# Optimization experiments

Hardware: AMD Instinct MI355X
Metric: run time of the kernel (lower is better)

Reference implementation:

```python
import jax, jax.numpy as jnp
import numpy as np

B, T, K = 128, 1024, 24
START_TAG, END_TAG = 22, 23


def setup_inputs() -> dict:
    key = jax.random.key(0)
    k1, k2, k3 = jax.random.split(key, 3)
    scores = jax.random.normal(k1, (B, T, K, K), dtype=jnp.float32)
    targets = jax.random.randint(k2, (B, T), 0, K * K)
    # lengths must be sorted descending (pack_padded_sequence convention), >= 1
    lengths = jnp.sort(jax.random.randint(k3, (B,), 1, T + 1))[::-1]
    return {"scores": scores, "targets": targets, "lengths": lengths}


def reference(scores, targets, lengths):
    b, t_len, k, _ = scores.shape
    # gold path score: gather targets from flattened [B,T,K*K] view, mask by length
    flat = scores.reshape(b, t_len, k * k)
    scores_at_targets = jnp.take_along_axis(flat, targets[:, :, None], axis=2)[..., 0]  # [B,T]
    time_mask = jnp.arange(t_len)[None, :] < lengths[:, None]  # [B,T]
    gold_score = jnp.sum(jnp.where(time_mask, scores_at_targets, 0.0))

    # CRF forward recursion (log-sum-exp over previous tag), sequential over time.
    # t == 0: initialize with row of the <start> tag (all lengths >= 1).
    prev = scores[:, 0, START_TAG, :]  # [B,K]

    def step(prev, inp):
        s_t, m_t = inp  # s_t: [B,K,K], m_t: [B] bool (t < length)
        new = jax.scipy.special.logsumexp(s_t + prev[:, :, None], axis=1)  # [B,K]
        prev = jnp.where(m_t[:, None], new, prev)
        return prev, None

    s_rest = jnp.moveaxis(scores[:, 1:], 0, 1)  # time-major [T-1,B,K,K]
    m_rest = jnp.arange(1, t_len)[:, None] < lengths[None, :]  # [T-1,B]
    prev, _ = jax.lax.scan(step, prev, (s_rest, m_rest))

    all_paths_scores = prev[:, END_TAG].sum()
    return (all_paths_scores - gold_score) / b
```

## Files before the change

### kernel.cpp

```cpp
#include <hip/hip_runtime.h>

static constexpr int T_LEN = 1024;
static constexpr int KTAG = 24;
static constexpr int MAT = 576;
static constexpr int START_TAG = 22;
static constexpr int END_TAG = 23;
static constexpr int BATCH = 128;
static constexpr int CHUNK = 32;
static constexpr int NCHUNK = 32;

static constexpr float LOG2E = 1.4426950408889634f;
static constexpr float LN2   = 0.6931471805599453f;

typedef short  bf16x8 __attribute__((ext_vector_type(8)));
typedef float  f32x16 __attribute__((ext_vector_type(16)));

__device__ __forceinline__ float fexp2(float x) { return __builtin_amdgcn_exp2f(x); }
__device__ __forceinline__ float flog2(float x) { return __builtin_amdgcn_logf(x); }

__device__ __forceinline__ unsigned int f2bf(float x) {
  unsigned int u = __float_as_uint(x);
  u += 0x7FFFu + ((u >> 16) & 1u);
  return u >> 16;
}

__global__ __launch_bounds__(256) void chunkprod_kernel(
    const float* __restrict__ scores, const int* __restrict__ targets,
    const int* __restrict__ lengths,
    float* __restrict__ wsP, int* __restrict__ wsE, float* __restrict__ wsG)
{
  const int widx = threadIdx.x >> 6;
  const int lane = threadIdx.x & 63;
  const int g = blockIdx.x * 4 + widx;
  const int b = (int)(__brev((unsigned)(g & 127)) >> 25);
  const int c = g >> 7;
  const int len = lengths[b];
  const int t0 = 1 + c * CHUNK;
  if (t0 >= len) return;
  const int n = min(CHUNK, len - t0);
  const int hd = lane >> 5;
  const int m = lane & 31;
  const int mc = m < KTAG ? m : KTAG - 1;
  const float* sb = scores + (size_t)b * T_LEN * MAT;

  {
    float gs = 0.f;
    if (lane < n) {
      int t = t0 + lane;
      gs = sb[(size_t)t * MAT + targets[b * T_LEN + t]];
    }
    #pragma unroll
    for (int off = 1; off < 64; off <<= 1) gs += __shfl_xor(gs, off, 64);
    if (lane == 0) wsG[b * NCHUNK + c] = gs;
  }

  int off1[8], off2[4];
  #pragma unroll
  for (int e = 0; e < 8; ++e) {
    int k = (e & 3) + 8 * (e >> 2) + 4 * hd;
    off1[e] = k * KTAG + mc;
  }
  #pragma unroll
  for (int e = 0; e < 4; ++e) {
    int k = 16 + e + 4 * hd;
    off2[e] = k * KTAG + mc;
  }

  float b0[12], b1[12], b2[12], b3[12];
  auto LOADA = [&](float (&buf)[12], int step) {
    const float* pb = sb + (size_t)(t0 + step) * MAT;
    #pragma unroll
    for (int e = 0; e < 8; ++e) buf[e] = pb[off1[e]];
    #pragma unroll
    for (int e = 0; e < 4; ++e) buf[8 + e] = pb[off2[e]];
  };

  unsigned int p[8];
  #pragma unroll
  for (int r = 0; r < 8; ++r) {
    int rlo = ((2 * r) & 3) + 8 * ((2 * r) >> 2) + 4 * hd;
    unsigned int v = 0;
    if (m == rlo)     v |= 0x3F80u;
    if (m == rlo + 1) v |= (0x3F80u << 16);
    p[r] = v;
  }

  int E = 0;

  auto STEPM = [&](const float (&buf)[12]) -> f32x16 {
    float av[12];
    #pragma unroll
    for (int i = 0; i < 12; ++i) av[i] = fexp2(buf[i] * LOG2E);
    bf16x8 a1, a2;
    #pragma unroll
    for (int e = 0; e < 8; ++e) a1[e] = (short)f2bf(av[e]);
    #pragma unroll
    for (int e = 0; e < 4; ++e) a2[e] = (short)f2bf(av[8 + e]);
    #pragma unroll
    for (int e = 4; e < 8; ++e) a2[e] = 0;
    union { unsigned int u[4]; bf16x8 v; } B1, B2;
    B1.u[0] = p[0]; B1.u[1] = p[1]; B1.u[2] = p[2]; B1.u[3] = p[3];
    B2.u[0] = p[4]; B2.u[1] = p[5]; B2.u[2] = p[6]; B2.u[3] = p[7];
    f32x16 d = {};
    d = __builtin_amdgcn_mfma_f32_32x32x16_bf16(a1, B1.v, d, 0, 0, 0);
    d = __builtin_amdgcn_mfma_f32_32x32x16_bf16(a2, B2.v, d, 0, 0, 0);
    return d;
  };

  auto CONV = [&](const f32x16& d) {
    int rb = __builtin_amdgcn_readfirstlane(__float_as_int(d[0]));
    int dd = ((rb >> 23) & 255) - 127;
    E += dd;
    float sc = __int_as_float((127 - dd) << 23);
    #pragma unroll
    for (int r = 0; r < 8; ++r)
      p[r] = (f2bf(d[2 * r + 1] * sc) << 16) | f2bf(d[2 * r] * sc);
  };

  LOADA(b0, 0);
  LOADA(b1, n > 1 ? 1 : 0);
  LOADA(b2, n > 2 ? 2 : 0);
  LOADA(b3, n > 3 ? 3 : 0);
  f32x16 z;
  int s = 0;
  for (;;) {
    z = STEPM(b0);
    if (s + 1 >= n) break;
    CONV(z); { int t = s + 4; LOADA(b0, t < n ? t : n - 1); }
    z = STEPM(b1);
    if (s + 2 >= n) break;
    CONV(z); { int t = s + 5; LOADA(b1, t < n ? t : n - 1); }
    z = STEPM(b2);
    if (s + 3 >= n) break;
    CONV(z); { int t = s + 6; LOADA(b2, t < n ? t : n - 1); }
    z = STEPM(b3);
    if (s + 4 >= n) break;
    CONV(z); { int t = s + 7; LOADA(b3, t < n ? t : n - 1); }
    s += 4;
  }

  if (m < KTAG) {
    float* dst = wsP + (size_t)(b * NCHUNK + c) * MAT + m * KTAG;
    float4 v0 = make_float4(z[0], z[1], z[2],  z[3]);
    float4 v1 = make_float4(z[4], z[5], z[6],  z[7]);
    float4 v2 = make_float4(z[8], z[9], z[10], z[11]);
    *(float4*)(dst + 4 * hd)      = v0;
    *(float4*)(dst + 8 + 4 * hd)  = v1;
    *(float4*)(dst + 16 + 4 * hd) = v2;
  }
  if (lane == 0) wsE[b * NCHUNK + c] = E;
}

__global__ __launch_bounds__(64) void chainvec_kernel(
    const float* __restrict__ scores, const int* __restrict__ targets,
    const float* __restrict__ wsP, const int* __restrict__ wsE,
    const float* __restrict__ wsG, const int* __restrict__ lengths,
    float* __restrict__ wsR)
{
  __shared__ float tau_s[32];
  volatile float* tau = tau_s;
  const int b = blockIdx.x;
  const int lane = threadIdx.x;
  const int h = lane >> 5;
  const int j = lane & 31;
  const int jj = j < KTAG ? j : KTAG - 1;
  const int len = lengths[b];
  const int nc = (len + 30) >> 5;

  if (lane < KTAG)
    tau[lane] = fexp2(scores[(size_t)b * T_LEN * MAT + START_TAG * KTAG + lane] * LOG2E);

  float gv = 0.f;
  if (lane < nc) gv = wsG[b * NCHUNK + lane];
  #pragma unroll
  for (int off = 1; off < 64; off <<= 1) gv += __shfl_xor(gv, off, 64);

  int E = 0;
  float wa[12], wb[12];

  auto LOADV = [&](float (&buf)[12], int c) {
    const float* p = wsP + (size_t)(b * NCHUNK + c) * MAT + (h * 12) * KTAG + jj;
    #pragma unroll
    for (int k = 0; k < 12; ++k) buf[k] = p[k * KTAG];
  };
  auto STEPV = [&](const float (&buf)[12], int c) {
    int ec = wsE[b * NCHUNK + c];
    const float4* tp = (const float4*)((const float*)&tau_s[h * 12]);
    float4 t0 = tp[0], t1 = tp[1], t2 = tp[2];
    float a0 = t0.x * buf[0], a1 = t0.y * buf[1], a2 = t0.z * buf[2], a3 = t0.w * buf[3];
    a0 = fmaf(t1.x, buf[4],  a0); a1 = fmaf(t1.y, buf[5],  a1);
    a2 = fmaf(t1.z, buf[6],  a2); a3 = fmaf(t1.w, buf[7],  a3);
    a0 = fmaf(t2.x, buf[8],  a0); a1 = fmaf(t2.y, buf[9],  a1);
    a2 = fmaf(t2.z, buf[10], a2); a3 = fmaf(t2.w, buf[11], a3);
    float part = (a0 + a1) + (a2 + a3);
    float tot = part + __shfl_xor(part, 32, 64);
    int rb = __builtin_amdgcn_readfirstlane(__float_as_int(tot));
    int d = ((rb >> 23) & 255) - 127;
    E += d + ec;
    float sc = __int_as_float((127 - d) << 23);
    if (lane < KTAG) tau[lane] = tot * sc;
  };

  if (nc > 0) {
    LOADV(wa, 0);
    LOADV(wb, nc > 1 ? 1 : 0);
    int c = 0;
    while (c + 1 < nc) {
      STEPV(wa, c);     { int t = c + 2; LOADV(wa, t < nc ? t : nc - 1); }
      STEPV(wb, c + 1); { int t = c + 3; LOADV(wb, t < nc ? t : nc - 1); }
      c += 2;
    }
    if (c < nc) STEPV(wa, c);
  }

  if (lane == 0) {
    float g0 = scores[(size_t)b * T_LEN * MAT + targets[b * T_LEN]];
    float logZ = ((float)E + flog2(tau[END_TAG])) * LN2;
    wsR[b] = logZ - gv - g0;
  }
}

__global__ __launch_bounds__(64) void sum_kernel(
    const float* __restrict__ wsR, float* __restrict__ out)
{
  const int lane = threadIdx.x;
  float v = wsR[lane] + wsR[lane + 64];
  #pragma unroll
  for (int off = 1; off < 64; off <<= 1) v += __shfl_xor(v, off, 64);
  if (lane == 0) out[0] = v * (1.0f / (float)BATCH);
}

template<int DIR>
__device__ __forceinline__ int run_chain(const float* __restrict__ base, int len, int n,
                                         volatile float* __restrict__ tau,
                                         int lane, int h, int jj)
{
  int E = 0;
  float ref = 1.0f;
  float A[12], B[12], Cb[12];
  auto LOAD = [&](float (&buf)[12], int i) {
    if (DIR == 0) {
      const float* p = base + (size_t)(1 + i) * MAT + h * 12 * KTAG + jj;
      #pragma unroll
      for (int k = 0; k < 12; ++k) buf[k] = p[k * KTAG];
    } else {
      const float4* p = (const float4*)(base + (size_t)(len - 1 - i) * MAT + jj * KTAG + h * 12);
      float4 x = p[0], y = p[1], z = p[2];
      buf[0]=x.x; buf[1]=x.y; buf[2]=x.z; buf[3]=x.w;
      buf[4]=y.x; buf[5]=y.y; buf[6]=y.z; buf[7]=y.w;
      buf[8]=z.x; buf[9]=z.y; buf[10]=z.z; buf[11]=z.w;
    }
  };
  auto STEP = [&](const float (&buf)[12]) {
    int rb = __builtin_amdgcn_readfirstlane(__float_as_int(ref));
    int d = ((rb >> 23) & 255) - 127;
    float sc = __int_as_float((127 - d) << 23);
    E += d;
    float w[12];
    #pragma unroll
    for (int k = 0; k < 12; ++k) w[k] = fexp2(buf[k] * LOG2E);
    const float4* tp = (const float4*)((const float*)&tau[h * 12]);
    float4 t0 = tp[0], t1 = tp[1], t2 = tp[2];
    float a0 = t0.x*w[0], a1 = t0.y*w[1], a2 = t0.z*w[2], a3 = t0.w*w[3];
    a0 = fmaf(t1.x, w[4],  a0); a1 = fmaf(t1.y, w[5],  a1);
    a2 = fmaf(t1.z, w[6],  a2); a3 = fmaf(t1.w, w[7],  a3);
    a0 = fmaf(t2.x, w[8],  a0); a1 = fmaf(t2.y, w[9],  a1);
    a2 = fmaf(t2.z, w[10], a2); a3 = fmaf(t2.w, w[11], a3);
    float part = (a0 + a1) + (a2 + a3);
    float tot = part + __shfl_xor(part, 32, 64);
    float tn = tot * sc;
    if (lane < KTAG) tau[lane] = tn;
    ref = tn;
  };
  if (n > 0) {
    LOAD(A, 0); LOAD(B, n > 1 ? 1 : 0); LOAD(Cb, n > 2 ? 2 : 0);
    int i = 0;
    while (i + 3 <= n) {
      STEP(A);  { int ii = i + 3; LOAD(A,  ii < n ? ii : n - 1); }
      STEP(B);  { int ii = i + 4; LOAD(B,  ii < n ? ii : n - 1); }
      STEP(Cb); { int ii = i + 5; LOAD(Cb, ii < n ? ii : n - 1); }
      i += 3;
    }
    if (i < n)     STEP(A);
    if (i + 1 < n) STEP(B);
  }
  return E;
}

__global__ __launch_bounds__(128) void crf_fb_kernel(
    const float* __restrict__ scores, const int* __restrict__ lengths,
    float* __restrict__ acc)
{
  __shared__ float sm[2][32];
  __shared__ int smE[2];
  const int b = blockIdx.x;
  const int tid = threadIdx.x;
  const int wid = tid >> 6;
  const int lane = tid & 63;
  const int h = lane >> 5;
  const int j = lane & 31;
  const int jj = j < KTAG ? j : KTAG - 1;
  const int len = lengths[b];
  const float* base = scores + (size_t)b * T_LEN * MAT;
  const int m = len >> 1;
  volatile float* tau = sm[wid];
  int E;
  if (wid == 0) {
    if (lane < KTAG) tau[lane] = fexp2(base[START_TAG * KTAG + lane] * LOG2E);
    E = run_chain<0>(base, len, m, tau, lane, h, jj);
  } else {
    if (lane < KTAG) tau[lane] = (lane == END_TAG) ? 1.0f : 0.0f;
    E = run_chain<1>(base, len, len - 1 - m, tau, lane, h, jj);
  }
  if (lane == 0) smE[wid] = E;
  __syncthreads();
  if (wid == 0) {
    float v = (lane < KTAG) ? sm[0][lane] * sm[1][lane] : 0.0f;
    #pragma unroll
    for (int off = 1; off < 32; off <<= 1) v += __shfl_xor(v, off, 64);
    if (lane == 0) {
      float res = ((float)(smE[0] + smE[1]) + flog2(v)) * LN2;
      atomicAdd(acc, res);
    }
  }
}

__global__ __launch_bounds__(256) void gold_kernel(
    const float* __restrict__ scores, const int* __restrict__ targets,
    const int* __restrict__ lengths, float* __restrict__ acc)
{
  const int idx = blockIdx.x * blockDim.x + threadIdx.x;
  const int b = idx >> 10;
  const int t = idx & (T_LEN - 1);
  float v = 0.f;
  if (t < lengths[b]) v = scores[(size_t)idx * MAT + targets[idx]];
  #pragma unroll
  for (int off = 1; off < 64; off <<= 1) v += __shfl_xor(v, off, 64);
  if ((threadIdx.x & 63) == 0) atomicAdd(acc, -v);
}

__global__ void finalize_kernel(const float* __restrict__ acc, float* __restrict__ out) {
  out[0] = acc[0] * (1.0f / (float)BATCH);
}

extern "C" void kernel_launch(void* const* d_in, const int* in_sizes, int n_in,
                              void* d_out, int out_size, void* d_ws, size_t ws_size,
                              hipStream_t stream) {
  const float* scores = (const float*)d_in[0];
  const int* targets  = (const int*)d_in[1];
  const int* lengths  = (const int*)d_in[2];
  float* out = (float*)d_out;

  const size_t pbytes = (size_t)BATCH * NCHUNK * MAT * sizeof(float);
  const size_t ebytes = (size_t)BATCH * NCHUNK * sizeof(int);
  const size_t gbytes = (size_t)BATCH * NCHUNK * sizeof(float);
  const size_t need = pbytes + ebytes + gbytes + BATCH * sizeof(float);

  if (ws_size >= need) {
    float* wsP = (float*)d_ws;
    int*   wsE = (int*)((char*)d_ws + pbytes);
    float* wsG = (float*)((char*)d_ws + pbytes + ebytes);
    float* wsR = (float*)((char*)d_ws + pbytes + ebytes + gbytes);
    chunkprod_kernel<<<BATCH * NCHUNK / 4, 256, 0, stream>>>(scores, targets, lengths,
                                                             wsP, wsE, wsG);
    chainvec_kernel<<<BATCH, 64, 0, stream>>>(scores, targets, wsP, wsE, wsG,
                                              lengths, wsR);
    sum_kernel<<<1, 64, 0, stream>>>(wsR, out);
  } else {
    float* acc = (float*)d_ws;
    hipMemsetAsync(acc, 0, sizeof(float), stream);
    gold_kernel<<<BATCH * T_LEN / 256, 256, 0, stream>>>(scores, targets, lengths, acc);
    crf_fb_kernel<<<BATCH, 128, 0, stream>>>(scores, lengths, acc);
    finalize_kernel<<<1, 1, 0, stream>>>(acc, out);
  }
}
```

Before: 68.79 us.

## Chain chunk transfer matrices with bf16 MFMA matrix products instead of vector steps

The second-stage kernel no longer propagates a vector through the chunk products with shared-memory broadcasts and FMAs. It now multiplies the full chunk matrices together using bf16 32x32x16 MFMA instructions, keeping the running product in registers, and applies the start vector only at the end. The goal is to remove the per-step LDS round trip and shuffle latency on the sequential chain. In exchange it does more arithmetic per step and rounds the intermediate products to bf16, which costs some accuracy.

```diff
diff --git a/kernel.cpp b/kernel.cpp
--- a/kernel.cpp
+++ b/kernel.cpp
@@ -151,71 +151,116 @@
   if (lane == 0) wsE[b * NCHUNK + c] = E;
 }
 
-__global__ __launch_bounds__(64) void chainvec_kernel(
+__global__ __launch_bounds__(64) void chainmat_kernel(
     const float* __restrict__ scores, const int* __restrict__ targets,
     const float* __restrict__ wsP, const int* __restrict__ wsE,
     const float* __restrict__ wsG, const int* __restrict__ lengths,
     float* __restrict__ wsR)
 {
-  __shared__ float tau_s[32];
-  volatile float* tau = tau_s;
   const int b = blockIdx.x;
   const int lane = threadIdx.x;
-  const int h = lane >> 5;
-  const int j = lane & 31;
-  const int jj = j < KTAG ? j : KTAG - 1;
+  const int hd = lane >> 5;
+  const int m = lane & 31;
+  const int mc = m < KTAG ? m : KTAG - 1;
   const int len = lengths[b];
   const int nc = (len + 30) >> 5;
-
-  if (lane < KTAG)
-    tau[lane] = fexp2(scores[(size_t)b * T_LEN * MAT + START_TAG * KTAG + lane] * LOG2E);
+  const float* sb = scores + (size_t)b * T_LEN * MAT;
 
   float gv = 0.f;
   if (lane < nc) gv = wsG[b * NCHUNK + lane];
   #pragma unroll
   for (int off = 1; off < 64; off <<= 1) gv += __shfl_xor(gv, off, 64);
-
-  int E = 0;
-  float wa[12], wb[12];
-
-  auto LOADV = [&](float (&buf)[12], int c) {
-    const float* p = wsP + (size_t)(b * NCHUNK + c) * MAT + (h * 12) * KTAG + jj;
-    #pragma unroll
-    for (int k = 0; k < 12; ++k) buf[k] = p[k * KTAG];
-  };
-  auto STEPV = [&](const float (&buf)[12], int c) {
-    int ec = wsE[b * NCHUNK + c];
-    const float4* tp = (const float4*)((const float*)&tau_s[h * 12]);
-    float4 t0 = tp[0], t1 = tp[1], t2 = tp[2];
-    float a0 = t0.x * buf[0], a1 = t0.y * buf[1], a2 = t0.z * buf[2], a3 = t0.w * buf[3];
-    a0 = fmaf(t1.x, buf[4],  a0); a1 = fmaf(t1.y, buf[5],  a1);
-    a2 = fmaf(t1.z, buf[6],  a2); a3 = fmaf(t1.w, buf[7],  a3);
-    a0 = fmaf(t2.x, buf[8],  a0); a1 = fmaf(t2.y, buf[9],  a1);
-    a2 = fmaf(t2.z, buf[10], a2); a3 = fmaf(t2.w, buf[11], a3);
-    float part = (a0 + a1) + (a2 + a3);
-    float tot = part + __shfl_xor(part, 32, 64);
-    int rb = __builtin_amdgcn_readfirstlane(__float_as_int(tot));
-    int d = ((rb >> 23) & 255) - 127;
-    E += d + ec;
-    float sc = __int_as_float((127 - d) << 23);
-    if (lane < KTAG) tau[lane] = tot * sc;
-  };
-
-  if (nc > 0) {
-    LOADV(wa, 0);
-    LOADV(wb, nc > 1 ? 1 : 0);
-    int c = 0;
-    while (c + 1 < nc) {
-      STEPV(wa, c);     { int t = c + 2; LOADV(wa, t < nc ? t : nc - 1); }
-      STEPV(wb, c + 1); { int t = c + 3; LOADV(wb, t < nc ? t : nc - 1); }
-      c += 2;
-    }
-    if (c < nc) STEPV(wa, c);
-  }
-
+  const float g0 = sb[targets[b * T_LEN]];
+
+  if (nc == 0) {
+    if (lane == 0) wsR[b] = sb[START_TAG * KTAG + END_TAG] - g0;
+    return;
+  }
+
+  int ev = 0;
+  if (lane < nc) ev = wsE[b * NCHUNK + lane];
+  #pragma unroll
+  for (int off = 1; off < 64; off <<= 1) ev += __shfl_xor(ev, off, 64);
+  int E = ev;
+
+  int off1[8], off2[4];
+  #pragma unroll
+  for (int e = 0; e < 8; ++e) {
+    int k = (e & 3) + 8 * (e >> 2) + 4 * hd;
+    off1[e] = k * KTAG + mc;
+  }
+  #pragma unroll
+  for (int e = 0; e < 4; ++e) {
+    int k = 16 + e + 4 * hd;
+    off2[e] = k * KTAG + mc;
+  }
+  const float* pbase = wsP + (size_t)b * NCHUNK * MAT;
+
+  float b0[12], b1[12];
+  auto LOADP = [&](float (&buf)[12], int c) {
+    const float* pb = pbase + (size_t)c * MAT;
+    #pragma unroll
+    for (int e = 0; e < 8; ++e) buf[e] = pb[off1[e]];
+    #pragma unroll
+    for (int e = 0; e < 4; ++e) buf[8 + e] = pb[off2[e]];
+  };
+
+  unsigned int p[8];
+  #pragma unroll
+  for (int r = 0; r < 8; ++r) {
+    int rlo = ((2 * r) & 3) + 8 * ((2 * r) >> 2) + 4 * hd;
+    unsigned int v = 0;
+    if (m == rlo)     v |= 0x3F80u;
+    if (m == rlo + 1) v |= (0x3F80u << 16);
+    p[r] = v;
+  }
+
+  auto STEPP = [&](const float (&buf)[12]) -> f32x16 {
+    bf16x8 a1, a2;
+    #pragma unroll
+    for (int e = 0; e < 8; ++e) a1[e] = (short)f2bf(buf[e]);
+    #pragma unroll
+    for (int e = 0; e < 4; ++e) a2[e] = (short)f2bf(buf[8 + e]);
+    #pragma unroll
+    for (int e = 4; e < 8; ++e) a2[e] = 0;
+    union { unsigned int u[4]; bf16x8 v; } B1, B2;
+    B1.u[0] = p[0]; B1.u[1] = p[1]; B1.u[2] = p[2]; B1.u[3] = p[3];
+    B2.u[0] = p[4]; B2.u[1] = p[5]; B2.u[2] = p[6]; B2.u[3] = p[7];
+    f32x16 d = {};
+    d = __builtin_amdgcn_mfma_f32_32x32x16_bf16(a1, B1.v, d, 0, 0, 0);
+    d = __builtin_amdgcn_mfma_f32_32x32x16_bf16(a2, B2.v, d, 0, 0, 0);
+    return d;
+  };
+  auto CONVP = [&](const f32x16& d) {
+    int rb = __builtin_amdgcn_readfirstlane(__float_as_int(d[0]));
+    int dd = ((rb >> 23) & 255) - 127;
+    E += dd;
+    float sc = __int_as_float((127 - dd) << 23);
+    #pragma unroll
+    for (int r = 0; r < 8; ++r)
+      p[r] = (f2bf(d[2 * r + 1] * sc) << 16) | f2bf(d[2 * r] * sc);
+  };
+
+  LOADP(b0, 0);
+  LOADP(b1, nc > 1 ? 1 : 0);
+  f32x16 z;
+  int c = 0;
+  for (;;) {
+    z = STEPP(b0);
+    if (c + 1 >= nc) break;
+    CONVP(z); { int t = c + 2; LOADP(b0, t < nc ? t : nc - 1); }
+    z = STEPP(b1);
+    if (c + 2 >= nc) break;
+    CONVP(z); { int t = c + 3; LOADP(b1, t < nc ? t : nc - 1); }
+    c += 2;
+  }
+
+  float tau0 = fexp2(sb[START_TAG * KTAG + mc] * LOG2E);
+  float v = (hd == 1 && m < KTAG) ? z[11] * tau0 : 0.f;
+  #pragma unroll
+  for (int off = 1; off < 64; off <<= 1) v += __shfl_xor(v, off, 64);
   if (lane == 0) {
-    float g0 = scores[(size_t)b * T_LEN * MAT + targets[b * T_LEN]];
-    float logZ = ((float)E + flog2(tau[END_TAG])) * LN2;
+    float logZ = ((float)E + flog2(v)) * LN2;
     wsR[b] = logZ - gv - g0;
   }
 }
@@ -363,7 +408,7 @@
     float* wsR = (float*)((char*)d_ws + pbytes + ebytes + gbytes);
     chunkprod_kernel<<<BATCH * NCHUNK / 4, 256, 0, stream>>>(scores, targets, lengths,
                                                              wsP, wsE, wsG);
-    chainvec_kernel<<<BATCH, 64, 0, stream>>>(scores, targets, wsP, wsE, wsG,
+    chainmat_kernel<<<BATCH, 64, 0, stream>>>(scores, targets, wsP, wsE, wsG,
                                               lengths, wsR);
     sum_kernel<<<1, 64, 0, stream>>>(wsR, out);
   } else {
```

Result: faster. 63.58 us (-7.6%).
